# Kernel tuning notes

Measured on AMD Instinct MI355X. Metric: run time of the kernel, lower is better.

Reference implementation:

```python
import jax, jax.numpy as jnp
import numpy as np

NUM_BUCKETS = 32
MAX_DISTANCE = 128
N_HEADS = 16
D_KV = 64


def relative_position_bucket(rel, num_buckets=NUM_BUCKETS, max_distance=MAX_DISTANCE):
    # bidirectional (encoder) bucketing, matches the torch reference
    nb = num_buckets // 2
    ret = (rel > 0).astype(jnp.int32) * nb
    rp = jnp.abs(rel)
    max_exact = nb // 2
    is_small = rp < max_exact
    # guard log(0); masked out by is_small anyway
    large = max_exact + (
        jnp.log(jnp.maximum(rp, 1).astype(jnp.float32) / max_exact)
        / np.log(max_distance / max_exact)
        * (nb - max_exact)
    ).astype(jnp.int32)
    large = jnp.minimum(large, nb - 1)
    return ret + jnp.where(is_small, rp, large)


def compute_bias(rel_bias_table, q_len, k_len):
    q_pos = jnp.arange(q_len)[:, None]
    k_pos = jnp.arange(k_len)[None, :]
    buckets = relative_position_bucket(k_pos - q_pos)  # [S, K]
    bias = rel_bias_table[buckets]                      # [S, K, H]
    return jnp.transpose(bias, (2, 0, 1))[None]         # [1, H, S, K]


def setup_inputs() -> dict:
    key = jax.random.key(0)
    ks = jax.random.split(key, 6)
    d_model, inner = 1024, N_HEADS * D_KV
    scale = 1.0 / np.sqrt(d_model)
    return {
        "hidden_states": jax.random.normal(ks[0], (4, 2048, d_model), jnp.float32),
        "Wq": jax.random.normal(ks[1], (d_model, inner), jnp.float32) * scale,
        "Wk": jax.random.normal(ks[2], (d_model, inner), jnp.float32) * scale,
        "Wv": jax.random.normal(ks[3], (d_model, inner), jnp.float32) * scale,
        "Wo": jax.random.normal(ks[4], (inner, d_model), jnp.float32) * scale,
        "rel_bias_table": jax.random.normal(ks[5], (NUM_BUCKETS, N_HEADS), jnp.float32),
    }


def reference(hidden_states, Wq, Wk, Wv, Wo, rel_bias_table):
    B, S, _ = hidden_states.shape
    K_len = S  # self-attention (key_value_states is None)
    q = (hidden_states @ Wq).reshape(B, S, N_HEADS, D_KV)
    k = (hidden_states @ Wk).reshape(B, K_len, N_HEADS, D_KV)
    v = (hidden_states @ Wv).reshape(B, K_len, N_HEADS, D_KV)
    # NOTE: T5 attention has no 1/sqrt(d_kv) scaling
    scores = jnp.einsum("bshd,bkhd->bhsk", q, k)
    pos_bias = compute_bias(rel_bias_table, S, K_len)
    attn = jax.nn.softmax(scores + pos_bias, axis=-1)
    out = jnp.einsum("bhsk,bkhd->bshd", attn, v).reshape(B, S, N_HEADS * D_KV)
    out = out @ Wo
    return (out, pos_bias)
```

## Files before the change

### kernel.cpp

```cpp
#include <hip/hip_runtime.h>
#include <cstdint>
#include <cstddef>

typedef unsigned short u16;
typedef unsigned int u32;
typedef __attribute__((ext_vector_type(8))) short bf16x8;
typedef __attribute__((ext_vector_type(4))) float f32x4;
typedef __attribute__((ext_vector_type(16))) float f32x16;

#define MFMA(a, b, c)   __builtin_amdgcn_mfma_f32_16x16x32_bf16((a), (b), (c), 0, 0, 0)
#define MFMA32(a, b, c) __builtin_amdgcn_mfma_f32_32x32x16_bf16((a), (b), (c), 0, 0, 0)

typedef const __attribute__((address_space(1))) void gv1_t;
typedef __attribute__((address_space(3))) void lv3_t;
#define GLOAD_LDS16(g, l) __builtin_amdgcn_global_load_lds((gv1_t*)(g), (lv3_t*)(l), 16, 0, 0)

#define BATCH 4
#define SEQ 2048
#define DMODEL 1024
#define NHEAD 16
#define MROWS (BATCH * SEQ)
#define QKVN (3 * DMODEL)

#define LOG2E 1.44269504088896340736f

__device__ __forceinline__ u16 f2bf(float f) {
  u32 x = __builtin_bit_cast(u32, f);
  x += 0x7fffu + ((x >> 16) & 1u);
  return (u16)(x >> 16);
}

__device__ __forceinline__ u32 pkbf(float a, float b) {
  return (u32)f2bf(a) | ((u32)f2bf(b) << 16);
}

extern "C" __device__ float __ocml_exp2_f32(float);
__device__ __forceinline__ float exp2fast(float x) {
#if __has_builtin(__builtin_amdgcn_exp2f)
  return __builtin_amdgcn_exp2f(x);
#else
  return __ocml_exp2_f32(x);
#endif
}

__global__ __launch_bounds__(256) void convert_h(const float* __restrict__ H,
                                                 u16* __restrict__ Hb) {
  size_t i = (size_t)blockIdx.x * 1024 + threadIdx.x * 4;
  float4 v = *(const float4*)&H[i];
  uint2 o;
  o.x = pkbf(v.x, v.y);
  o.y = pkbf(v.z, v.w);
  *(uint2*)&Hb[i] = o;
}

__global__ void transpose_w(const float* __restrict__ Wq, const float* __restrict__ Wk,
                            const float* __restrict__ Wv, const float* __restrict__ Wo,
                            u16* __restrict__ Wt) {
  __shared__ u16 Ts[32][33];
  const float* W = (blockIdx.z == 0) ? Wq : (blockIdx.z == 1) ? Wk
                   : (blockIdx.z == 2) ? Wv : Wo;
  const float s = (blockIdx.z == 0) ? LOG2E : 1.0f;
  int x = threadIdx.x, y0 = threadIdx.y;
  int r0 = blockIdx.y * 32, c0 = blockIdx.x * 32;
  for (int yy = y0; yy < 32; yy += 8)
    Ts[yy][x] = f2bf(W[(size_t)(r0 + yy) * 1024 + c0 + x] * s);
  __syncthreads();
  for (int yy = y0; yy < 32; yy += 8)
    Wt[(size_t)(blockIdx.z * 1024 + c0 + yy) * 1024 + r0 + x] = Ts[x][yy];
}

__device__ __forceinline__ int rel_bucket(int rel) {
  int ret = (rel > 0) ? 16 : 0;
  int rp = (rel < 0) ? -rel : rel;
  if (rp < 8) return ret + rp;
  int i = 0;
  i += (rp >= 12); i += (rp >= 16); i += (rp >= 23); i += (rp >= 32);
  i += (rp >= 46); i += (rp >= 64); i += (rp >= 91);
  return ret + 8 + i;
}

__global__ __launch_bounds__(256) void build_bias_rel(const float* __restrict__ tbl,
                                                      float* __restrict__ brel,
                                                      float* __restrict__ brel2) {
  int h = blockIdx.x;
  for (int rix = threadIdx.x; rix < 4095; rix += 256) {
    float v = tbl[rel_bucket(rix - 2047) * NHEAD + h];
    brel[h * 4096 + rix] = v;
    brel2[h * 4096 + rix] = v * LOG2E;
  }
}

__global__ __launch_bounds__(256) void gemm_bf16k(const u16* __restrict__ A,
                                                  const u16* __restrict__ Bt,
                                                  u16* __restrict__ Cb, float* __restrict__ Cf,
                                                  int M, int N, int K) {
  __shared__ u16 As[128 * 32];
  __shared__ u16 Bs[128 * 32];
  const int t = threadIdx.x;
  const int w = t >> 6, lane = t & 63, quad = lane >> 4, l15 = lane & 15;
  const int wr = w >> 1, wc = w & 1;
  const int row0 = blockIdx.y * 128, col0 = blockIdx.x * 128;

  f32x4 acc[4][4];
  #pragma unroll
  for (int i = 0; i < 4; ++i)
    #pragma unroll
    for (int j = 0; j < 4; ++j) acc[i][j] = (f32x4){0.f, 0.f, 0.f, 0.f};

  const int srow = lane >> 2, scol = (lane & 3) * 8;

  for (int k0 = 0; k0 < K; k0 += 32) {
    #pragma unroll
    for (int p = 0; p < 2; ++p) {
      const int rb = w * 32 + p * 16;
      GLOAD_LDS16(&A[(size_t)(row0 + rb + srow) * K + k0 + scol], &As[rb * 32]);
      GLOAD_LDS16(&Bt[(size_t)(col0 + rb + srow) * K + k0 + scol], &Bs[rb * 32]);
    }
    __syncthreads();
    bf16x8 af[4], bfr[4];
    #pragma unroll
    for (int i = 0; i < 4; ++i)
      af[i] = *(const bf16x8*)&As[(wr * 64 + i * 16 + l15) * 32 + quad * 8];
    #pragma unroll
    for (int j = 0; j < 4; ++j)
      bfr[j] = *(const bf16x8*)&Bs[(wc * 64 + j * 16 + l15) * 32 + quad * 8];
    #pragma unroll
    for (int i = 0; i < 4; ++i)
      #pragma unroll
      for (int j = 0; j < 4; ++j)
        acc[i][j] = MFMA(af[i], bfr[j], acc[i][j]);
    __syncthreads();
  }
  #pragma unroll
  for (int i = 0; i < 4; ++i) {
    #pragma unroll
    for (int j = 0; j < 4; ++j) {
      int col = col0 + wc * 64 + j * 16 + l15;
      #pragma unroll
      for (int r = 0; r < 4; ++r) {
        int row = row0 + wr * 64 + i * 16 + quad * 4 + r;
        if (Cb) Cb[(size_t)row * N + col] = f2bf(acc[i][j][r]);
        else    Cf[(size_t)row * N + col] = acc[i][j][r];
      }
    }
  }
}

__global__ __launch_bounds__(256) void transpose_v(const u16* __restrict__ QKV,
                                                   u16* __restrict__ Vt) {
  __shared__ u16 Ts[64 * 72];
  int st = blockIdx.x, bh = blockIdx.y;
  int b = bh >> 4, h = bh & 15;
  int t = threadIdx.x;
  #pragma unroll
  for (int p = 0; p < 2; ++p) {
    int c = t * 2 + p, r = c >> 3, cc = (c & 7) * 8;
    *(uint4*)&Ts[r * 72 + cc] =
        *(const uint4*)&QKV[(size_t)(b * SEQ + st * 64 + r) * QKVN + 2 * DMODEL + h * 64 + cc];
  }
  __syncthreads();
  #pragma unroll
  for (int p = 0; p < 2; ++p) {
    int c = t * 2 + p, d = c >> 3, s8 = (c & 7) * 8;
    union { u16 u[8]; uint4 v; } tmp;
    #pragma unroll
    for (int jj = 0; jj < 8; ++jj) tmp.u[jj] = Ts[(s8 + jj) * 72 + d];
    *(uint4*)&Vt[((size_t)(bh * 64 + d)) * SEQ + st * 64 + s8] = tmp.v;
  }
}

__global__ __launch_bounds__(256) void attn_fused(const u16* __restrict__ QKV,
                                                  const u16* __restrict__ Vt,
                                                  const float* __restrict__ brel,
                                                  const float* __restrict__ brel2,
                                                  u16* __restrict__ Aout,
                                                  float* __restrict__ pb) {
  __shared__ u16 Ks[64 * 72];
  __shared__ u16 Vs[64 * 72];
  __shared__ u16 Ps[4][32 * 72];
  const int qt = blockIdx.x, bh = blockIdx.y;
  const int b = bh >> 4, h = bh & 15;
  const int t = threadIdx.x;
  const int w = t >> 6, lane = t & 63, l31 = lane & 31, h5 = lane >> 5;
  const int qb = qt * 128;
  const int qw0 = qb + w * 32;
  const int qr = qw0 + l31;
  const bool wrbias = (bh < 16);

  const float cpos = brel2[h * 4096 + 4040];
  const float cneg = brel2[h * 4096 + 54];
  const float cpu  = brel[h * 4096 + 4040];
  const float cnu  = brel[h * 4096 + 54];

  const u16* qptr = QKV + (size_t)(b * SEQ + qr) * QKVN + h * 64 + h5 * 8;
  bf16x8 qf[4];
  #pragma unroll
  for (int ks = 0; ks < 4; ++ks) qf[ks] = *(const bf16x8*)(qptr + ks * 16);

  float lsum = 0.f;
  f32x16 oacc[2];
  #pragma unroll
  for (int m = 0; m < 2; ++m)
    #pragma unroll
    for (int i = 0; i < 16; ++i) oacc[m][i] = 0.f;

  const int c0 = t * 2, c1 = c0 + 1;
  const int r0s = c0 >> 3, cc0 = (c0 & 7) * 8;
  const int r1s = c1 >> 3, cc1 = (c1 & 7) * 8;
  const size_t krow = (size_t)(b * SEQ) * QKVN + DMODEL + h * 64;
  const size_t vtrow = (size_t)bh * 64;
  const float* brow = brel2 + h * 4096 + 2047;
  u16* Pw = Ps[w];

  uint4 ka0 = *(const uint4*)&QKV[krow + (size_t)r0s * QKVN + cc0];
  uint4 ka1 = *(const uint4*)&QKV[krow + (size_t)r1s * QKVN + cc1];
  uint4 va0 = *(const uint4*)&Vt[(vtrow + r0s) * SEQ + cc0];
  uint4 va1 = *(const uint4*)&Vt[(vtrow + r1s) * SEQ + cc1];

  for (int kb = 0; kb < SEQ; kb += 64) {
    *(uint4*)&Ks[r0s * 72 + cc0] = ka0;
    *(uint4*)&Ks[r1s * 72 + cc1] = ka1;
    *(uint4*)&Vs[r0s * 72 + cc0] = va0;
    *(uint4*)&Vs[r1s * 72 + cc1] = va1;
    __syncthreads();

    if (kb + 64 < SEQ) {
      ka0 = *(const uint4*)&QKV[krow + (size_t)(kb + 64 + r0s) * QKVN + cc0];
      ka1 = *(const uint4*)&QKV[krow + (size_t)(kb + 64 + r1s) * QKVN + cc1];
      va0 = *(const uint4*)&Vt[(vtrow + r0s) * SEQ + kb + 64 + cc0];
      va1 = *(const uint4*)&Vt[(vtrow + r1s) * SEQ + kb + 64 + cc1];
    }

    f32x16 sc[2];
    #pragma unroll
    for (int m = 0; m < 2; ++m) {
      #pragma unroll
      for (int i = 0; i < 16; ++i) sc[m][i] = 0.f;
      #pragma unroll
      for (int ks = 0; ks < 4; ++ks) {
        bf16x8 kf = *(const bf16x8*)&Ks[(m * 32 + l31) * 72 + ks * 16 + h5 * 8];
        sc[m] = MFMA32(kf, qf[ks], sc[m]);
      }
    }

    if (wrbias) {
      const int pr = qb + (t >> 1);
      const int pc = kb + (t & 1) * 32;
      float* po = pb + ((size_t)(h * SEQ + pr)) * SEQ + pc;
      const int lo = pc - pr;
      if (lo >= 91 || lo + 31 <= -91) {
        const float c = (lo >= 91) ? cpu : cnu;
        const float4 vv = {c, c, c, c};
        #pragma unroll
        for (int i = 0; i < 8; ++i) *(float4*)&po[i * 4] = vv;
      } else {
        const float* bb = brel + h * 4096 + 2047 - pr + pc;
        #pragma unroll
        for (int i = 0; i < 8; ++i) {
          float4 vv;
          vv.x = bb[i * 4]; vv.y = bb[i * 4 + 1];
          vv.z = bb[i * 4 + 2]; vv.w = bb[i * 4 + 3];
          *(float4*)&po[i * 4] = vv;
        }
      }
    }

    #pragma unroll
    for (int m = 0; m < 2; ++m) {
      const int kb32 = kb + 32 * m;
      if (kb32 >= qw0 + 122) {
        #pragma unroll
        for (int i = 0; i < 16; ++i) sc[m][i] += cpos;
      } else if (kb32 <= qw0 - 122) {
        #pragma unroll
        for (int i = 0; i < 16; ++i) sc[m][i] += cneg;
      } else {
        const float* bb = brow + kb32 + 4 * h5 - qr;
        #pragma unroll
        for (int i = 0; i < 16; ++i) sc[m][i] += bb[(i & 3) + 8 * (i >> 2)];
      }
      #pragma unroll
      for (int tt = 0; tt < 4; ++tt) {
        float p0 = exp2fast(sc[m][4 * tt + 0]);
        float p1 = exp2fast(sc[m][4 * tt + 1]);
        float p2 = exp2fast(sc[m][4 * tt + 2]);
        float p3 = exp2fast(sc[m][4 * tt + 3]);
        lsum += (p0 + p1) + (p2 + p3);
        uint2 pk;
        pk.x = pkbf(p0, p1);
        pk.y = pkbf(p2, p3);
        *(uint2*)&Pw[l31 * 72 + 32 * m + 8 * tt + 4 * h5] = pk;
      }
    }

    asm volatile("s_waitcnt lgkmcnt(0)" ::: "memory");
    bf16x8 bp[4];
    #pragma unroll
    for (int ks = 0; ks < 4; ++ks)
      bp[ks] = *(const bf16x8*)&Pw[l31 * 72 + ks * 16 + h5 * 8];
    #pragma unroll
    for (int m2 = 0; m2 < 2; ++m2)
      #pragma unroll
      for (int ks = 0; ks < 4; ++ks) {
        bf16x8 vf = *(const bf16x8*)&Vs[(m2 * 32 + l31) * 72 + ks * 16 + h5 * 8];
        oacc[m2] = MFMA32(vf, bp[ks], oacc[m2]);
      }
    __syncthreads();
  }

  lsum += __shfl_xor(lsum, 32);
  const float inv = 1.0f / lsum;
  const size_t rowb = (size_t)(b * SEQ + qr) * DMODEL + h * 64;
  #pragma unroll
  for (int m2 = 0; m2 < 2; ++m2)
    #pragma unroll
    for (int tt = 0; tt < 4; ++tt) {
      uint2 o;
      o.x = pkbf(oacc[m2][4 * tt + 0] * inv, oacc[m2][4 * tt + 1] * inv);
      o.y = pkbf(oacc[m2][4 * tt + 2] * inv, oacc[m2][4 * tt + 3] * inv);
      *(uint2*)&Aout[rowb + 32 * m2 + 8 * tt + 4 * h5] = o;
    }
}

extern "C" void kernel_launch(void* const* d_in, const int* in_sizes, int n_in,
                              void* d_out, int out_size, void* d_ws, size_t ws_size,
                              hipStream_t stream) {
  (void)in_sizes; (void)n_in; (void)out_size; (void)ws_size;
  const float* H   = (const float*)d_in[0];
  const float* Wq  = (const float*)d_in[1];
  const float* Wk  = (const float*)d_in[2];
  const float* Wv  = (const float*)d_in[3];
  const float* Wo  = (const float*)d_in[4];
  const float* tbl = (const float*)d_in[5];

  float* out = (float*)d_out;
  float* pos_bias = out + (size_t)MROWS * DMODEL;

  char* ws = (char*)d_ws;
  u16* Hb     = (u16*)(ws);
  u16* Wt     = (u16*)(ws + 16777216);
  u16* QKV    = (u16*)(ws + 25165824);
  u16* Vt     = (u16*)(ws + 75497472);
  float* brel  = (float*)(ws + 92274688);
  float* brel2 = (float*)(ws + 92536832);

  convert_h<<<8192, 256, 0, stream>>>(H, Hb);
  transpose_w<<<dim3(32, 32, 4), dim3(32, 8), 0, stream>>>(Wq, Wk, Wv, Wo, Wt);
  build_bias_rel<<<16, 256, 0, stream>>>(tbl, brel, brel2);

  gemm_bf16k<<<dim3(QKVN / 128, MROWS / 128), 256, 0, stream>>>(
      Hb, Wt, QKV, nullptr, MROWS, QKVN, DMODEL);
  transpose_v<<<dim3(32, 64), 256, 0, stream>>>(QKV, Vt);
  attn_fused<<<dim3(16, 64), 256, 0, stream>>>(QKV, Vt, brel, brel2,
                                               Hb , pos_bias);
  gemm_bf16k<<<dim3(DMODEL / 128, MROWS / 128), 256, 0, stream>>>(
      Hb, Wt + (size_t)QKVN * DMODEL, nullptr, out, MROWS, DMODEL, DMODEL);
}
```

Baseline: 603.4 us.

## Pass P through register shuffles instead of LDS and interleave QK/PV per half

Drops the per-wave LDS staging buffer for the softmax probabilities. The bf16 P fragments are now exchanged between lane halves with cross-lane xor shuffles and fed straight into the PV MFMAs. The QK score computation moves inside the per-32-key loop, so only one score accumulator is live at a time, and launch bounds request 3 blocks per CU. This cuts LDS traffic and footprint and lowers register pressure to allow more occupancy. The cost is extra shuffle instructions and possible register spilling under the tighter bound.

```diff
diff --git a/kernel.cpp b/kernel.cpp
--- a/kernel.cpp
+++ b/kernel.cpp
@@ -169,15 +169,14 @@
   }
 }
 
-__global__ __launch_bounds__(256) void attn_fused(const u16* __restrict__ QKV,
-                                                  const u16* __restrict__ Vt,
-                                                  const float* __restrict__ brel,
-                                                  const float* __restrict__ brel2,
-                                                  u16* __restrict__ Aout,
-                                                  float* __restrict__ pb) {
+__global__ __launch_bounds__(256, 3) void attn_fused(const u16* __restrict__ QKV,
+                                                     const u16* __restrict__ Vt,
+                                                     const float* __restrict__ brel,
+                                                     const float* __restrict__ brel2,
+                                                     u16* __restrict__ Aout,
+                                                     float* __restrict__ pb) {
   __shared__ u16 Ks[64 * 72];
   __shared__ u16 Vs[64 * 72];
-  __shared__ u16 Ps[4][32 * 72];
   const int qt = blockIdx.x, bh = blockIdx.y;
   const int b = bh >> 4, h = bh & 15;
   const int t = threadIdx.x;
@@ -210,7 +209,6 @@
   const size_t krow = (size_t)(b * SEQ) * QKVN + DMODEL + h * 64;
   const size_t vtrow = (size_t)bh * 64;
   const float* brow = brel2 + h * 4096 + 2047;
-  u16* Pw = Ps[w];
 
   uint4 ka0 = *(const uint4*)&QKV[krow + (size_t)r0s * QKVN + cc0];
   uint4 ka1 = *(const uint4*)&QKV[krow + (size_t)r1s * QKVN + cc1];
@@ -229,18 +227,6 @@
       ka1 = *(const uint4*)&QKV[krow + (size_t)(kb + 64 + r1s) * QKVN + cc1];
       va0 = *(const uint4*)&Vt[(vtrow + r0s) * SEQ + kb + 64 + cc0];
       va1 = *(const uint4*)&Vt[(vtrow + r1s) * SEQ + kb + 64 + cc1];
-    }
-
-    f32x16 sc[2];
-    #pragma unroll
-    for (int m = 0; m < 2; ++m) {
-      #pragma unroll
-      for (int i = 0; i < 16; ++i) sc[m][i] = 0.f;
-      #pragma unroll
-      for (int ks = 0; ks < 4; ++ks) {
-        bf16x8 kf = *(const bf16x8*)&Ks[(m * 32 + l31) * 72 + ks * 16 + h5 * 8];
-        sc[m] = MFMA32(kf, qf[ks], sc[m]);
-      }
     }
 
     if (wrbias) {
@@ -267,44 +253,58 @@
 
     #pragma unroll
     for (int m = 0; m < 2; ++m) {
+      f32x16 sc;
+      #pragma unroll
+      for (int i = 0; i < 16; ++i) sc[i] = 0.f;
+      #pragma unroll
+      for (int ks = 0; ks < 4; ++ks) {
+        bf16x8 kf = *(const bf16x8*)&Ks[(m * 32 + l31) * 72 + ks * 16 + h5 * 8];
+        sc = MFMA32(kf, qf[ks], sc);
+      }
+
       const int kb32 = kb + 32 * m;
       if (kb32 >= qw0 + 122) {
         #pragma unroll
-        for (int i = 0; i < 16; ++i) sc[m][i] += cpos;
+        for (int i = 0; i < 16; ++i) sc[i] += cpos;
       } else if (kb32 <= qw0 - 122) {
         #pragma unroll
-        for (int i = 0; i < 16; ++i) sc[m][i] += cneg;
+        for (int i = 0; i < 16; ++i) sc[i] += cneg;
       } else {
         const float* bb = brow + kb32 + 4 * h5 - qr;
         #pragma unroll
-        for (int i = 0; i < 16; ++i) sc[m][i] += bb[(i & 3) + 8 * (i >> 2)];
-      }
+        for (int i = 0; i < 16; ++i) sc[i] += bb[(i & 3) + 8 * (i >> 2)];
+      }
+      uint2 pk[4], opk[4];
       #pragma unroll
       for (int tt = 0; tt < 4; ++tt) {
-        float p0 = exp2fast(sc[m][4 * tt + 0]);
-        float p1 = exp2fast(sc[m][4 * tt + 1]);
-        float p2 = exp2fast(sc[m][4 * tt + 2]);
-        float p3 = exp2fast(sc[m][4 * tt + 3]);
+        float p0 = exp2fast(sc[4 * tt + 0]);
+        float p1 = exp2fast(sc[4 * tt + 1]);
+        float p2 = exp2fast(sc[4 * tt + 2]);
+        float p3 = exp2fast(sc[4 * tt + 3]);
         lsum += (p0 + p1) + (p2 + p3);
-        uint2 pk;
-        pk.x = pkbf(p0, p1);
-        pk.y = pkbf(p2, p3);
-        *(uint2*)&Pw[l31 * 72 + 32 * m + 8 * tt + 4 * h5] = pk;
-      }
-    }
-
-    asm volatile("s_waitcnt lgkmcnt(0)" ::: "memory");
-    bf16x8 bp[4];
-    #pragma unroll
-    for (int ks = 0; ks < 4; ++ks)
-      bp[ks] = *(const bf16x8*)&Pw[l31 * 72 + ks * 16 + h5 * 8];
-    #pragma unroll
-    for (int m2 = 0; m2 < 2; ++m2)
-      #pragma unroll
-      for (int ks = 0; ks < 4; ++ks) {
-        bf16x8 vf = *(const bf16x8*)&Vs[(m2 * 32 + l31) * 72 + ks * 16 + h5 * 8];
-        oacc[m2] = MFMA32(vf, bp[ks], oacc[m2]);
-      }
+        pk[tt].x = pkbf(p0, p1);
+        pk[tt].y = pkbf(p2, p3);
+      }
+      #pragma unroll
+      for (int tt = 0; tt < 4; ++tt) {
+        opk[tt].x = (u32)__shfl_xor((int)pk[tt].x, 32);
+        opk[tt].y = (u32)__shfl_xor((int)pk[tt].y, 32);
+      }
+      #pragma unroll
+      for (int j = 0; j < 2; ++j) {
+        const int a = 2 * j;
+        uint2 lo_h = h5 ? opk[a + 1] : pk[a];
+        uint2 up_h = h5 ? pk[a + 1] : opk[a];
+        uint4 f = {lo_h.x, lo_h.y, up_h.x, up_h.y};
+        bf16x8 bp = __builtin_bit_cast(bf16x8, f);
+        const int ks = 2 * m + j;
+        #pragma unroll
+        for (int m2 = 0; m2 < 2; ++m2) {
+          bf16x8 vf = *(const bf16x8*)&Vs[(m2 * 32 + l31) * 72 + ks * 16 + h5 * 8];
+          oacc[m2] = MFMA32(vf, bp, oacc[m2]);
+        }
+      }
+    }
     __syncthreads();
   }
 
```

Result: no change. 609.5 us (+1.0%).
